# Kernel optimization log

Measured on AMD Instinct MI355X. Metric: run time of the kernel, lower is better.

The kernel has to match this reference:

```python
import jax, jax.numpy as jnp
import numpy as np

KSIZE = 7
STRIDE = 4
SCALE = 10.0
C_IN = 64
C_INT = 16
TOP_M = 100


def _unfold(x, k, s):
    # x: [B,C,H,W] -> [B, C*k*k, L] with torch.nn.Unfold channel ordering (c, ki, kj)
    B, C, H, W = x.shape
    oh = (H - k) // s + 1
    ow = (W - k) // s + 1
    rows = jnp.arange(oh)[:, None] * s + jnp.arange(k)[None, :]  # [oh,k]
    cols = jnp.arange(ow)[:, None] * s + jnp.arange(k)[None, :]  # [ow,k]
    p = x[:, :, rows][:, :, :, :, cols]          # [B,C,oh,k,ow,k]
    p = p.transpose(0, 1, 3, 5, 2, 4)            # [B,C,k,k,oh,ow]
    return p.reshape(B, C * k * k, oh * ow)


def _fold(p, H, W, k, s):
    # inverse of _unfold with overlap-add (torch.nn.Fold semantics)
    B, D, L = p.shape
    C = D // (k * k)
    oh = (H - k) // s + 1
    ow = (W - k) // s + 1
    rows = jnp.arange(oh)[:, None] * s + jnp.arange(k)[None, :]
    cols = jnp.arange(ow)[:, None] * s + jnp.arange(k)[None, :]
    p = p.reshape(B, C, k, k, oh, ow).transpose(0, 1, 4, 2, 5, 3)  # [B,C,oh,k,ow,k]
    out = jnp.zeros((B, C, H, W), p.dtype)
    return out.at[:, :, rows[:, :, None, None], cols[None, None, :, :]].add(p)


def _conv1x1(x, w, b):
    return jnp.einsum('bchw,oc->bohw', x, w) + b[None, :, None, None]


def _conv3x3(x, w, b):
    y = jax.lax.conv_general_dilated(x, w, (1, 1), ((1, 1), (1, 1)),
                                     dimension_numbers=('NCHW', 'OIHW', 'NCHW'))
    return y + b[None, :, None, None]


def setup_inputs() -> dict:
    key = jax.random.key(0)
    ks = jax.random.split(key, 12)
    B, H, W = 4, 127, 127
    s = 0.05  # small init std keeps softmax logits in a sane range
    return {
        'x': jax.random.normal(ks[0], (B, C_IN, H, W), jnp.float32),
        'g_w': jax.random.normal(ks[1], (C_INT, C_IN, 3, 3), jnp.float32) * s,
        'g_b': jnp.zeros((C_INT,), jnp.float32),
        'theta_w': jax.random.normal(ks[2], (C_INT, C_IN), jnp.float32) * s,
        'theta_b': jnp.zeros((C_INT,), jnp.float32),
        'phi_w': jax.random.normal(ks[3], (C_INT, C_IN), jnp.float32) * s,
        'phi_b': jnp.zeros((C_INT,), jnp.float32),
        'match_w': jax.random.normal(ks[4], (C_INT, C_IN), jnp.float32) * s,
        'match_b': jnp.zeros((C_INT,), jnp.float32),
        'restore_w': jax.random.normal(ks[5], (C_IN, C_INT), jnp.float32) * s,
        'restore_b': jnp.zeros((C_IN,), jnp.float32),
    }


def reference(x, g_w, g_b, theta_w, theta_b, phi_w, phi_b,
              match_w, match_b, restore_w, restore_b):
    B, C, H, W = x.shape
    b1 = _conv3x3(x, g_w, g_b)           # [B,16,H,W]
    b2 = _conv1x1(x, theta_w, theta_b)
    b3 = _conv1x1(x, phi_w, phi_b)

    p1 = _unfold(b1, KSIZE, STRIDE).transpose(0, 2, 1)  # [B,L,D], D=16*49
    p2 = _unfold(b2, KSIZE, STRIDE).transpose(0, 2, 1)
    p3 = _unfold(b3, KSIZE, STRIDE).transpose(0, 2, 1)

    score = jnp.einsum('bld,bmd->blm', p1, p2)           # [B,L,L]
    L = score.shape[-1]
    k = min(TOP_M, L)
    vals, idx = jax.lax.top_k(score, k)                  # [B,L,k]
    bI = jnp.arange(B)[:, None, None]
    rI = jnp.arange(L)[None, :, None]
    sparse = jnp.zeros_like(score).at[bI, rI, idx].set(vals)
    attn = jax.nn.softmax(sparse * SCALE, axis=-1)

    agg = jnp.einsum('blm,bmd->bld', attn, p3).transpose(0, 2, 1)  # [B,D,L]
    out = _fold(agg, H, W, KSIZE, STRIDE)                # [B,16,H,W]

    mask = _fold(_unfold(jnp.ones_like(x), KSIZE, STRIDE), H, W, KSIZE, STRIDE)
    mask = _conv1x1(mask, match_w, match_b)              # [B,16,H,W]

    out = out / (mask + 1e-8)
    out = _conv1x1(out, restore_w, restore_b)            # [B,64,H,W]
    return out
```

## Files before the change

### kernel.cpp

```cpp
#include <hip/hip_runtime.h>
#include <hip/hip_bf16.h>

typedef __hip_bfloat16 bf16;
typedef unsigned short ushort_t;
typedef __attribute__((ext_vector_type(8))) __bf16 bfv8;
typedef __attribute__((ext_vector_type(16))) float f32x16;

#define B_   4
#define CIN  64
#define CI   16
#define H_   127
#define W_   127
#define HW   (H_*W_)
#define KS   7
#define ST   4
#define OH_  31
#define L_   961
#define D_   784
#define TOPM 100

#define N1   1032256
#define WG_O 4
#define WT_O (WG_O + 9216)
#define WP_O (WT_O + 1024)
#define BG_O (WP_O + 1024)
#define BT_O (BG_O + 16)
#define BP_O (BT_O + 16)
#define SM_O (BP_O + 16)
#define SB_O (SM_O + 16)
#define RW_O (SB_O + 16)
#define RB_O (RW_O + 1024)
#define B1_O 12448
#define S3_O (B1_O + 3*N1)
#define WB_O (S3_O + B_*D_)
#define REG_O (WB_O + 36864)
#define SROW 964
#define SCSLOT 926464
#define AGSZ 753424
#define TKROW 112
#define SLST 72
#define PKPLANE 753424
#define PKSTR   1506848
#define PADW 129
#define PADPIX (PADW*PADW)
#define XPB  (PADPIX*64)
#define XPU  ((size_t)B_ * XPB)
#define PLANES_FL 4260096
#define PK_O (REG_O + PLANES_FL)

#define FULL_BYTES ((size_t)(PK_O + 3013696) * 4)
#define MID_BYTES  ((size_t)(REG_O + PLANES_FL) * 4)

__device__ __forceinline__ float bf2f(bf16 v) { return __bfloat162float(v); }
__device__ __forceinline__ float bflo(unsigned u) { return __uint_as_float(u << 16); }
__device__ __forceinline__ float bfhi(unsigned u) { return __uint_as_float(u & 0xFFFF0000u); }

template <typename T> struct Ld;
template <> struct Ld<float> {
  static __device__ __forceinline__ float f(const void* p, int i) { return ((const float*)p)[i]; }
};
template <> struct Ld<bf16> {
  static __device__ __forceinline__ float f(const void* p, int i) { return bf2f(((const bf16*)p)[i]); }
};

__device__ __forceinline__ unsigned fmap(float f) {
// ... 13 lines not shown
  h = f2bf(x);
  float hf = __uint_as_float(((unsigned)h) << 16);
  l = f2bf(x - hf);
}

#define LDW(ptr, i) (f ? ((const float*)(ptr))[i] : bf2f(((const bf16*)(ptr))[i]))
__global__ __launch_bounds__(256) void k_prep(
    const void* __restrict__ x,
    const void* g_w, const void* t_w, const void* p_w,
    const void* g_b, const void* t_b, const void* p_b,
    const void* m_w, const void* m_b, const void* r_w, const void* r_b,
    float* __restrict__ ws,
    ushort_t* __restrict__ xhh, ushort_t* __restrict__ xhl)
{
  __shared__ int sflag;
  {
    const unsigned short* xh = (const unsigned short*)x;
    if (threadIdx.x < 64) {
      int c = 0;
#pragma unroll
      for (int j = 0; j < 2; ++j) {
        unsigned u = xh[threadIdx.x * 2 + j];
        unsigned e = (u >> 7) & 0xFF;
        if (e >= 134) c++;
      }
#pragma unroll
      for (int o = 32; o; o >>= 1) c += __shfl_down(c, o);
      if (threadIdx.x == 0) sflag = (c >= 8) ? 1 : 0;
    }
  }
// ... 36 lines not shown
  }
  if (xhh) {
    const int4 z = make_int4(0, 0, 0, 0);
    for (int idx = gid; idx < B_ * 512 * 8; idx += gs) {
      int q = idx & 7, t = idx >> 3;
      int bp = t & 511, bb = t >> 9;
      int pp;
      if (bp < 129) pp = bp;
      else if (bp < 258) pp = 128 * PADW + (bp - 129);
      else if (bp < 385) pp = (bp - 257) * PADW;
      else pp = (bp - 384) * PADW + 128;
      size_t off = ((size_t)bb * PADPIX + pp) * 64 + q * 8;
      *(int4*)(xhh + off) = z;
      *(int4*)(xhl + off) = z;
    }
  }
}

__global__ __launch_bounds__(256) void k_hwc(
    const int* __restrict__ flag, const void* __restrict__ x,
    ushort_t* __restrict__ xhh, ushort_t* __restrict__ xhl)
{
  __shared__ float tile[64][65];
  int pix0 = blockIdx.x * 64;
  int tid = threadIdx.x;
  int g = tid >> 6, p = tid & 63;
  int pix = pix0 + p;
  bool ok = pix < B_ * HW;
  int bb = ok ? pix / HW : 0;
  int r  = ok ? pix - bb * HW : 0;
  if (*flag) {
    const float* xf = (const float*)x;
    for (int c = g * 16; c < g * 16 + 16; ++c)
      tile[p][c] = ok ? xf[((size_t)bb * CIN + c) * HW + r] : 0.f;
  } else {
    const bf16* xb = (const bf16*)x;
    for (int c = g * 16; c < g * 16 + 16; ++c)
      tile[p][c] = ok ? bf2f(xb[((size_t)bb * CIN + c) * HW + r]) : 0.f;
  }
  __syncthreads();
  int c2 = tid & 63, pg = tid >> 6;
  int pix2 = pix0 + pg * 16;
  int bb2 = pix2 / HW, r2 = pix2 - bb2 * HW;
  int h2 = r2 / W_, w2 = r2 - h2 * W_;
  for (int k = 0; k < 16; ++k) {
    if (pix2 + k < B_ * HW) {
      ushort_t h, l; splitbf(tile[pg * 16 + k][c2], h, l);
      size_t off = ((size_t)bb2 * PADPIX + (size_t)(h2 + 1) * PADW + (w2 + 1)) * 64 + c2;
      xhh[off] = h;
      xhl[off] = l;
    }
    if (++w2 == W_) { w2 = 0; if (++h2 == H_) { h2 = 0; ++bb2; } }
  }
}

__global__ __launch_bounds__(256) void k_conv3(
    const float* __restrict__ ws,
    const ushort_t* __restrict__ xhh, const ushort_t* __restrict__ xhl,
    ushort_t* __restrict__ b1h, ushort_t* __restrict__ b1l,
    ushort_t* __restrict__ b2h, ushort_t* __restrict__ b2l,
    ushort_t* __restrict__ b3, ushort_t* __restrict__ pk)
{
  __shared__ ushort_t sAh[128 * SLST], sAl[128 * SLST];
  __shared__ ushort_t sBh[64 * SLST],  sBl[64 * SLST];
  int bz = blockIdx.z;
  int h = blockIdx.x;
  int tid = threadIdx.x, lane = tid & 63, wv = tid >> 6;
  int grp = lane >> 3, ch = lane & 7;

  const ushort_t* xplane = ((wv == 0) ? xhh : xhl) + (size_t)bz * XPB;
  const ushort_t* wBh_ = (const ushort_t*)(ws + WB_O);
  const ushort_t* bsrc = (wv == 2) ? wBh_ : (wBh_ + 9 * 64 * 64);
  ushort_t* dplane = (wv == 0) ? sAh : (wv == 1) ? sAl : (wv == 2) ? sBh : sBl;

  int fr = lane & 31, kh = (lane >> 5) << 3;
  int mt = (wv >> 1) << 1;
// ... 59 lines not shown
      acc1 = __builtin_amdgcn_mfma_f32_32x32x16_bf16(ah1, bh, acc1, 0, 0, 0);
    }
  }
#undef LC
#undef LC_A
#undef LC_W
#undef WC
#undef WC_A
#undef WC_W

  int nw = ((wv & 1) << 5) + fr;
  if (pk) {
    __syncthreads();
    ushort_t* sb1h = sAh;
    ushort_t* sb1l = sAl;
#pragma unroll
    for (int s = 0; s < 2; ++s) {
      int mbase = (mt + s) * 32;
#pragma unroll
      for (int r = 0; r < 16; ++r) {
        int m = mbase + (r & 3) + ((r >> 2) << 3) + ((lane >> 5) << 2);
        float val = s ? acc1[r] : acc0[r];
        if (nw < 16) {
          ushort_t h2, l2; splitbf(val + ws[BG_O + nw], h2, l2);
          sb1h[m * 16 + nw] = h2; sb1l[m * 16 + nw] = l2;
        } else if (m < W_) {
          size_t ob = ((size_t)bz * HW + h * W_ + m) * 16;
          if (nw < 32) {
            int o = nw - 16; ushort_t h2, l2; splitbf(val + ws[BT_O + o], h2, l2);
            b2h[ob + o] = h2; b2l[ob + o] = l2;
          } else if (nw < 48) {
            int o = nw - 32; b3[ob + o] = f2bf(val + ws[BP_O + o]);
          }
        }
      }
    }
    __syncthreads();
    ushort_t* pkb = pk + (size_t)bz * PKSTR;
    int slh_lo = (h >= 6) ? ((h - 3) >> 2) : 0;
    int slh_hi = h >> 2; if (slh_hi > 30) slh_hi = 30;
    for (int slh = slh_lo; slh <= slh_hi; ++slh) {
      int nki = h - 4 * slh;
      size_t rb = ((size_t)nki * 961 + slh * 31) * 112;
      for (int t = tid; t < 31 * 14; t += 256) {
        int slw = t / 14, q = t - slw * 14;
        int m = slw * 4 + (q >> 1);
        int c0 = (q & 1) << 3;
        int4 vh = *(int4*)(sb1h + m * 16 + c0);
        int4 vl = *(int4*)(sb1l + m * 16 + c0);
        size_t doff = rb + (size_t)slw * 112 + q * 8;
        *(int4*)(pkb + doff)           = vh;
        *(int4*)(pkb + PKPLANE + doff) = vl;
      }
    }
  } else {
#pragma unroll
    for (int s = 0; s < 2; ++s) {
      int mbase = (mt + s) * 32;
#pragma unroll
      for (int r = 0; r < 16; ++r) {
        int m = mbase + (r & 3) + ((r >> 2) << 3) + ((lane >> 5) << 2);
        if (m >= W_) continue;
        size_t ob = ((size_t)bz * HW + h * W_ + m) * 16;
        float val = s ? acc1[r] : acc0[r];
        if (nw < 16) {
          ushort_t h2, l2; splitbf(val + ws[BG_O + nw], h2, l2);
          b1h[ob + nw] = h2; b1l[ob + nw] = l2;
// ... 94 lines not shown
    int lh = l / OH_, lw = l % OH_;
    s += bflo((unsigned)B3[((lh * ST + ki) * W_ + lw * ST + kj) * CI + c]);
  }
  red[chunk][c] = s;
  __syncthreads();
  if (threadIdx.x < 16) {
    float t = 0.f;
#pragma unroll
    for (int k = 0; k < 16; ++k) t += red[k][threadIdx.x];
    S3[(b * 49 + pos) * 16 + threadIdx.x] = t;
  }
}

__global__ __launch_bounds__(256) void k_pack(
    const ushort_t* __restrict__ b1h, const ushort_t* __restrict__ b1l,
    ushort_t* __restrict__ pk, int b0, unsigned pkstride_z)
{
  int idx = blockIdx.x * 256 + threadIdx.x;
  if (idx >= 961 * 98) return;
  int row = idx / 98, rem = idx - row * 98;
  int nki = rem / 14, q = rem - nki * 14;
  int slh = row / OH_, slw = row - slh * OH_;
  int src = ((slh * ST) * W_ + slw * ST + nki * W_) * 16 + q * 8;
  int dst = (nki * 961 + row) * 112 + q * 8;
  int batch = b0 + blockIdx.y;
  size_t poff = (size_t)batch * HW * CI;
  ushort_t* pkb = pk + (size_t)blockIdx.y * pkstride_z;
  *(int4*)(pkb + dst)           = *(const int4*)(b1h + poff + src);
  *(int4*)(pkb + PKPLANE + dst) = *(const int4*)(b1l + poff + src);
}

__global__ __launch_bounds__(256) void k_score(
    const ushort_t* __restrict__ b2h, const ushort_t* __restrict__ b2l,
    const ushort_t* __restrict__ pk,
    float* __restrict__ scb, int b0, unsigned scstride_z, unsigned pkstride_z)
{
  __shared__ ushort_t sAh[128 * SLST], sAl[128 * SLST];
  __shared__ ushort_t sBh[64 * SLST],  sBl[64 * SLST];
  int batch = b0 + blockIdx.z;
  size_t poff_g = (size_t)batch * HW * CI;
  float* Sc = scb + (size_t)blockIdx.z * scstride_z;

  int tid = threadIdx.x;
  int m0 = blockIdx.y * 128, n0 = blockIdx.x * 64;
  int lane = tid & 63;
  int wv = tid >> 6;
  int grp = lane >> 3, ch = lane & 7;

  const ushort_t* pkb = pk + (size_t)blockIdx.z * pkstride_z + (size_t)(wv & 1) * PKPLANE;

  int srow = n0 + lane;  if (srow > L_ - 1) srow = L_ - 1;
  int slh = srow / OH_, slw = srow - slh * OH_;
  int sbase = (slh * ST) * W_ + slw * ST;
  const ushort_t* splane = (wv == 2) ? (b2h + poff_g) : (b2l + poff_g);
  ushort_t* dplane = (wv == 0) ? sAh : (wv == 1) ? sAl : (wv == 2) ? sBh : sBl;
  ushort_t* drowB = dplane + lane * SLST;

  int fr = lane & 31;
  int kh = (lane >> 5) << 3;
  int mt = (wv >> 1) << 1;
  int aoff0 = (mt * 32 + fr) * SLST + kh;
  int aoff1 = ((mt + 1) * 32 + fr) * SLST + kh;
  int boff  = (((wv & 1) << 5) + fr) * SLST + kh;

  f32x16 acc0 = {0.f,0.f,0.f,0.f,0.f,0.f,0.f,0.f,0.f,0.f,0.f,0.f,0.f,0.f,0.f,0.f};
  f32x16 acc1 = {0.f,0.f,0.f,0.f,0.f,0.f,0.f,0.f,0.f,0.f,0.f,0.f,0.f,0.f,0.f,0.f};

  int4 pv0, pv1, pv2, pv3, pv4, pv5, pv6, pv7;
  int4 pv8, pv9, pv10, pv11, pv12, pv13, pv14, pv15;

#define LA(j) pv##j = *(const int4*)(pks + (size_t)min(m0 + 8*j + grp, 960) * 112)
#define LA_ALL LA(0); LA(1); LA(2); LA(3); LA(4); LA(5); LA(6); LA(7); \
               LA(8); LA(9); LA(10); LA(11); LA(12); LA(13); LA(14); LA(15)
#define WA(j) *(int4*)(d0 + (j) * 8 * SLST) = pv##j
#define WA_ALL WA(0); WA(1); WA(2); WA(3); WA(4); WA(5); WA(6); WA(7); \
               WA(8); WA(9); WA(10); WA(11); WA(12); WA(13); WA(14); WA(15)

  if (wv < 2) {
    const ushort_t* pks = pkb + ch * 8;
    LA_ALL;
  } else {
    const int4* s0 = (const int4*)(splane + (size_t)sbase * 16);
    pv0 = s0[0]; pv1 = s0[1]; pv2 = s0[2]; pv3 = s0[3];
    pv4 = s0[4]; pv5 = s0[5]; pv6 = s0[6]; pv7 = s0[7];
  }

  for (int r = 0; r < 14; ++r) {
    int half = r & 1;
    __syncthreads();
    if (wv < 2) {
      ushort_t* d0 = dplane + grp * SLST + ch * 8;
      if (!half) { WA_ALL; }
      else if (ch < 6) { WA_ALL; }
    } else {
      *(int4*)(drowB + 0)  = pv0;  *(int4*)(drowB + 8)  = pv1;
      *(int4*)(drowB + 16) = pv2;  *(int4*)(drowB + 24) = pv3;
      *(int4*)(drowB + 32) = pv4;  *(int4*)(drowB + 40) = pv5;
      if (!half) { *(int4*)(drowB + 48) = pv6; *(int4*)(drowB + 56) = pv7; }
    }
    __syncthreads();
    if (r < 13) {
      int rn = r + 1;
      int nki = rn >> 1, odd = rn & 1;
      if (wv < 2) {
        const ushort_t* pks = pkb + (size_t)nki * (961 * 112) + odd * 64 + ch * 8;
        if (!odd) { LA_ALL; }
        else if (ch < 6) { LA_ALL; }
      } else {
        int nkj0 = odd * 4;
        const int4* s0 = (const int4*)(splane + (size_t)(sbase + nki * W_ + nkj0) * 16);
        pv0 = s0[0]; pv1 = s0[1]; pv2 = s0[2]; pv3 = s0[3]; pv4 = s0[4]; pv5 = s0[5];
        if (!odd) { pv6 = s0[6]; pv7 = s0[7]; }
      }
    }
    if (!half) {
#pragma unroll
      for (int t = 0; t < 4; ++t) {
        bfv8 ah0 = *(const bfv8*)(sAh + aoff0 + t * 16);
        bfv8 al0 = *(const bfv8*)(sAl + aoff0 + t * 16);
        bfv8 ah1 = *(const bfv8*)(sAh + aoff1 + t * 16);
        bfv8 al1 = *(const bfv8*)(sAl + aoff1 + t * 16);
        bfv8 bh  = *(const bfv8*)(sBh + boff + t * 16);
        bfv8 bl  = *(const bfv8*)(sBl + boff + t * 16);
        acc0 = __builtin_amdgcn_mfma_f32_32x32x16_bf16(al0, bh, acc0, 0, 0, 0);
        acc0 = __builtin_amdgcn_mfma_f32_32x32x16_bf16(ah0, bl, acc0, 0, 0, 0);
        acc0 = __builtin_amdgcn_mfma_f32_32x32x16_bf16(ah0, bh, acc0, 0, 0, 0);
        acc1 = __builtin_amdgcn_mfma_f32_32x32x16_bf16(al1, bh, acc1, 0, 0, 0);
        acc1 = __builtin_amdgcn_mfma_f32_32x32x16_bf16(ah1, bl, acc1, 0, 0, 0);
// ... 6 lines not shown
        bfv8 al0 = *(const bfv8*)(sAl + aoff0 + t * 16);
        bfv8 ah1 = *(const bfv8*)(sAh + aoff1 + t * 16);
        bfv8 al1 = *(const bfv8*)(sAl + aoff1 + t * 16);
        bfv8 bh  = *(const bfv8*)(sBh + boff + t * 16);
        bfv8 bl  = *(const bfv8*)(sBl + boff + t * 16);
        acc0 = __builtin_amdgcn_mfma_f32_32x32x16_bf16(al0, bh, acc0, 0, 0, 0);
        acc0 = __builtin_amdgcn_mfma_f32_32x32x16_bf16(ah0, bl, acc0, 0, 0, 0);
        acc0 = __builtin_amdgcn_mfma_f32_32x32x16_bf16(ah0, bh, acc0, 0, 0, 0);
        acc1 = __builtin_amdgcn_mfma_f32_32x32x16_bf16(al1, bh, acc1, 0, 0, 0);
        acc1 = __builtin_amdgcn_mfma_f32_32x32x16_bf16(ah1, bl, acc1, 0, 0, 0);
        acc1 = __builtin_amdgcn_mfma_f32_32x32x16_bf16(ah1, bh, acc1, 0, 0, 0);
      }
    }
  }
#undef LA
#undef LA_ALL
#undef WA
#undef WA_ALL

  int nw = n0 + ((wv & 1) << 5) + fr;
  if (nw < L_) {
    int mw0 = m0 + mt * 32;
#pragma unroll
    for (int r = 0; r < 16; ++r) {
      int m = mw0 + (r & 3) + ((r >> 2) << 3) + ((lane >> 5) << 2);
      if (m < L_) Sc[(size_t)m * SROW + nw] = acc0[r];
    }
    int mw1 = m0 + (mt + 1) * 32;
#pragma unroll
    for (int r = 0; r < 16; ++r) {
      int m = mw1 + (r & 3) + ((r >> 2) << 3) + ((lane >> 5) << 2);
      if (m < L_) Sc[(size_t)m * SROW + nw] = acc1[r];
    }
  }
}

__global__ __launch_bounds__(256) void k_topk(
    const float* __restrict__ scb, float* __restrict__ tkw, int* __restrict__ tkp,
    unsigned scstride_z)
{
  __shared__ float swv[4][TOPM];
  __shared__ int spx[4][TOPM];
  int tid = threadIdx.x;
  int wvi = tid >> 6, lane = tid & 63;
  int l = blockIdx.x * 4 + wvi;
  if (l > L_ - 1) l = L_ - 1;
  int bz = blockIdx.y;
  const float4* row4 = (const float4*)(scb + (size_t)bz * scstride_z + (size_t)l * SROW);
  int trow = (bz * L_ + l) * TKROW;

  unsigned k[16];
#pragma unroll
  for (int q = 0; q < 4; ++q) {
    float4 v = row4[q * 64 + lane];
    int ib = (q * 64 + lane) * 4;
    k[q * 4 + 0] = (ib + 0 < L_) ? fmap(v.x) : 0u;
    k[q * 4 + 1] = (ib + 1 < L_) ? fmap(v.y) : 0u;
    k[q * 4 + 2] = (ib + 2 < L_) ? fmap(v.z) : 0u;
    k[q * 4 + 3] = (ib + 3 < L_) ? fmap(v.w) : 0u;
  }

  unsigned mk = 0;
#pragma unroll
  for (int r = 0; r < 16; ++r) mk = max(mk, k[r]);
#pragma unroll
  for (int o = 32; o; o >>= 1) mk = max(mk, (unsigned)__shfl_down((int)mk, o));
  mk = (unsigned)__shfl((int)mk, 0);
  float vmax = unfmap(mk);

  unsigned kk[16];
#pragma unroll
  for (int r = 0; r < 16; ++r) kk[r] = k[r];

  unsigned prefix = 0; int base = 0;
  for (int bit = 30; bit >= 0; bit -= 2) {
    int n3 = 0, n2 = 0, n1 = 0;
#pragma unroll
    for (int r = 0; r < 16; ++r) {
      unsigned f = (kk[r] >> bit) & 3u;
      n3 += (int)__popcll(__ballot(f == 3u));
      n2 += (int)__popcll(__ballot(f >= 2u));
      n1 += (int)__popcll(__ballot(f >= 1u));
    }
    unsigned ch;
    if (base + n3 >= TOPM) ch = 3;
    else if (base + n2 >= TOPM) { ch = 2; base += n3; }
    else if (base + n1 >= TOPM) { ch = 1; base += n2; }
    else { ch = 0; base += n1; }
    prefix |= ch << bit;
#pragma unroll
    for (int r = 0; r < 16; ++r) {
      unsigned f = (kk[r] >> bit) & 3u;
      kk[r] = (f == ch) ? kk[r] : 0u;
    }
  }
  int nA = base;
  int needT = TOPM - nA;

  int cA = 0, cT = 0;
#pragma unroll
  for (int r = 0; r < 16; ++r) { cA += (k[r] > prefix); cT += (k[r] == prefix); }
  int pk = cA | (cT << 16);
  int incl = pk;
#pragma unroll
  for (int o = 1; o < 64; o <<= 1) { int t = __shfl_up(incl, o); if (lane >= o) incl += t; }
  int excl = incl - pk;
  int tA = excl & 0xFFFF, tT = excl >> 16;

  float M = fmaxf(10.f * vmax, 0.f);
  float e0 = __expf(-M);
  float z = 0.f;
#pragma unroll
  for (int r = 0; r < 16; ++r) {
    unsigned kr = k[r];
    int slot = -1;
    if (kr > prefix) slot = tA++;
    else if (kr == prefix) { if (tT < needT) slot = nA + tT; tT++; }
    if (slot >= 0) {
      float v = unfmap(kr);
      float wv = __expf(10.f * v - M);
      swv[wvi][slot] = wv; z += wv;
      int gi = 256 * (r >> 2) + 4 * lane + (r & 3);
      int lh = gi / OH_, lw = gi - lh * OH_;
      spx[wvi][slot] = ((lh * ST) * W_ + lw * ST) * CI;
    }
  }
#pragma unroll
  for (int o = 32; o; o >>= 1) z += __shfl_down(z, o);
  z = __shfl(z, 0);
  float Z = z + (float)(L_ - TOPM) * e0;
  float invZ = 1.f / Z;
  float w0 = e0 / Z;
  __syncthreads();
#pragma unroll
  for (int s0 = 0; s0 < 2; ++s0) {
    int s = lane + 64 * s0;
    if (s < TOPM) {
      tkw[trow + s] = swv[wvi][s] * invZ - w0;
      tkp[trow + s] = spx[wvi][s];
    }
  }
  if (lane == 0) tkw[trow + TOPM] = w0;
}

__global__ __launch_bounds__(128) void k_pv(
    const float* __restrict__ tkw, const int* __restrict__ tkp,
    const ushort_t* __restrict__ b3, const float* __restrict__ s3,
    float* __restrict__ agb, int b0, unsigned agstride_z)
{
  int l = blockIdx.x, bz = blockIdx.y;
  int batch = b0 + bz;
  int trow = (bz * L_ + l) * TKROW;
  const ushort_t* B3 = b3 + (size_t)batch * HW * CI;
  const float* S3 = s3 + (size_t)batch * D_;
  float* agg = agb + (size_t)bz * agstride_z;
  int tid = threadIdx.x;
  if (tid >= 98) return;

  float w0 = tkw[trow + TOPM];
  int pos = tid >> 1;
  int c0 = (tid & 1) << 3;
  int ki = pos / 7, kj = pos - (pos / 7) * 7;
  int poff = (ki * W_ + kj) * CI + c0;

  float a0 = 0.f, a1 = 0.f, a2 = 0.f, a3 = 0.f;
  float a4 = 0.f, a5 = 0.f, a6 = 0.f, a7 = 0.f;
  for (int j0 = 0; j0 < TOPM; j0 += 4) {
    float w_0 = tkw[trow + j0 + 0];
    float w_1 = tkw[trow + j0 + 1];
    float w_2 = tkw[trow + j0 + 2];
    float w_3 = tkw[trow + j0 + 3];
    int p_0 = tkp[trow + j0 + 0];
    int p_1 = tkp[trow + j0 + 1];
    int p_2 = tkp[trow + j0 + 2];
    int p_3 = tkp[trow + j0 + 3];
    const uint4 q0 = *(const uint4*)(B3 + p_0 + poff);
    const uint4 q1 = *(const uint4*)(B3 + p_1 + poff);
    const uint4 q2 = *(const uint4*)(B3 + p_2 + poff);
    const uint4 q3 = *(const uint4*)(B3 + p_3 + poff);
    a0 += w_0 * bflo(q0.x); a1 += w_0 * bfhi(q0.x); a2 += w_0 * bflo(q0.y); a3 += w_0 * bfhi(q0.y);
    a4 += w_0 * bflo(q0.z); a5 += w_0 * bfhi(q0.z); a6 += w_0 * bflo(q0.w); a7 += w_0 * bfhi(q0.w);
    a0 += w_1 * bflo(q1.x); a1 += w_1 * bfhi(q1.x); a2 += w_1 * bflo(q1.y); a3 += w_1 * bfhi(q1.y);
    a4 += w_1 * bflo(q1.z); a5 += w_1 * bfhi(q1.z); a6 += w_1 * bflo(q1.w); a7 += w_1 * bfhi(q1.w);
    a0 += w_2 * bflo(q2.x); a1 += w_2 * bfhi(q2.x); a2 += w_2 * bflo(q2.y); a3 += w_2 * bfhi(q2.y);
    a4 += w_2 * bflo(q2.z); a5 += w_2 * bfhi(q2.z); a6 += w_2 * bflo(q2.w); a7 += w_2 * bfhi(q2.w);
    a0 += w_3 * bflo(q3.x); a1 += w_3 * bfhi(q3.x); a2 += w_3 * bflo(q3.y); a3 += w_3 * bfhi(q3.y);
    a4 += w_3 * bflo(q3.z); a5 += w_3 * bfhi(q3.z); a6 += w_3 * bflo(q3.w); a7 += w_3 * bfhi(q3.w);
  }
  const float4 s40 = *(const float4*)(S3 + tid * 8);
  const float4 s41 = *(const float4*)(S3 + tid * 8 + 4);
// ... 91 lines not shown

  float* W = (float*)d_ws;
  int* flag = (int*)d_ws;
  ushort_t* planes = (ushort_t*)(W + B1_O);
  ushort_t* b1h = planes;
  ushort_t* b1l = planes + (size_t)N1;
  ushort_t* b2h = planes + (size_t)2 * N1;
  ushort_t* b2l = planes + (size_t)3 * N1;
  ushort_t* b3  = planes + (size_t)4 * N1;
  float* s3 = W + S3_O;

  if (ws_size >= FULL_BYTES) {
    ushort_t* xhh = (ushort_t*)(W + REG_O);
    ushort_t* xhl = xhh + XPU;
    float* sc = W + REG_O;
    ushort_t* pk = (ushort_t*)(W + PK_O);
    float* ag = W + PK_O;
    float* tkw = W + B1_O + N1;
    int*   tkp = (int*)(W + B1_O + N1 + N1 / 2);
    k_prep<<<64, 256, 0, stream>>>(x, g_w, th_w, ph_w, g_b, th_b, ph_b,
                                   m_w, m_b, r_w, r_b, W, xhh, xhl);
    k_hwc<<<dim3((B_ * HW + 63) / 64), 256, 0, stream>>>(flag, x, xhh, xhl);
    k_conv3<<<dim3(H_, 1, B_), 256, 0, stream>>>(
        W, xhh, xhl, b1h, b1l, b2h, b2l, b3, pk);
    k_colsum<<<dim3(B_, 49), 256, 0, stream>>>(b3, s3);
    k_score<<<dim3(16, 8, B_), 256, 0, stream>>>(b2h, b2l, pk, sc, 0, SCSLOT, PKSTR);
    k_topk<<<dim3((L_ + 3) / 4, B_), 256, 0, stream>>>(sc, tkw, tkp, SCSLOT);
    k_pv<<<dim3(L_, B_), 128, 0, stream>>>(tkw, tkp, b3, s3, ag, 0, AGSZ);
    k_fold<<<dim3(64, B_), 256, 0, stream>>>(flag, W, ag, d_out, 0, AGSZ);
  } else if (ws_size >= MID_BYTES) {
    ushort_t* xhh = (ushort_t*)(W + REG_O);
    ushort_t* xhl = xhh + XPU;
    float* sc = W + REG_O;
    float* ag = W + REG_O + SCSLOT;
    ushort_t* pk = (ushort_t*)ag;
    k_prep<<<64, 256, 0, stream>>>(x, g_w, th_w, ph_w, g_b, th_b, ph_b,
                                   m_w, m_b, r_w, r_b, W, xhh, xhl);
    k_hwc<<<dim3((B_ * HW + 63) / 64), 256, 0, stream>>>(flag, x, xhh, xhl);
    k_conv3<<<dim3(H_, 1, B_), 256, 0, stream>>>(
        W, xhh, xhl, b1h, b1l, b2h, b2l, b3, (ushort_t*)nullptr);
    k_colsum<<<dim3(B_, 49), 256, 0, stream>>>(b3, s3);
    for (int b = 0; b < B_; ++b) {
      float* tkw = W + B1_O + N1 + (size_t)b * (HW * CI / 2);
      int*   tkp = (int*)(W + B1_O + N1 + N1 / 2 + (size_t)b * (HW * CI / 2));
      k_pack<<<dim3(368, 1), 256, 0, stream>>>(b1h, b1l, pk, b, 0);
      k_score<<<dim3(16, 8, 1), 256, 0, stream>>>(b2h, b2l, pk, sc, b, 0, 0);
      k_topk<<<dim3((L_ + 3) / 4, 1), 256, 0, stream>>>(sc, tkw, tkp, 0);
      k_pv<<<dim3(L_, 1), 128, 0, stream>>>(tkw, tkp, b3, s3, ag, b, 0);
      k_fold<<<dim3(64, 1), 256, 0, stream>>>(flag, W, ag, d_out, b, 0);
    }
  } else {
    float* sc = W + REG_O;
    float* ag = W + REG_O + SCSLOT;
    ushort_t* pk = (ushort_t*)ag;
    k_prep<<<64, 256, 0, stream>>>(x, g_w, th_w, ph_w, g_b, th_b, ph_b,
                                   m_w, m_b, r_w, r_b, W,
                                   (ushort_t*)nullptr, (ushort_t*)nullptr);
    k_convF<<<dim3(4, 16, B_), dim3(32, 8, 1), 0, stream>>>(
        flag, x, g_w, g_b, th_w, th_b, ph_w, ph_b, b1h, b1l, b2h, b2l, b3);
    k_colsum<<<dim3(B_, 49), 256, 0, stream>>>(b3, s3);
    for (int b = 0; b < B_; ++b) {
      float* tkw = W + B1_O + N1 + (size_t)b * (HW * CI / 2);
      int*   tkp = (int*)(W + B1_O + N1 + N1 / 2 + (size_t)b * (HW * CI / 2));
      k_pack<<<dim3(368, 1), 256, 0, stream>>>(b1h, b1l, pk, b, 0);
      k_score<<<dim3(16, 8, 1), 256, 0, stream>>>(b2h, b2l, pk, sc, b, 0, 0);
      k_topk<<<dim3((L_ + 3) / 4, 1), 256, 0, stream>>>(sc, tkw, tkp, 0);
      k_pv<<<dim3(L_, 1), 128, 0, stream>>>(tkw, tkp, b3, s3, ag, b, 0);
      k_fold<<<dim3(64, 1), 256, 0, stream>>>(flag, W, ag, d_out, b, 0);
    }
  }
}
```

Baseline: 255.6 us.

## Fuse topk with PV, pre-pack theta patches, merge HWC transpose into prep

Merges the top-k selection and the weighted patch aggregation into one kernel that keeps the weights and indices in shared memory instead of round-tripping them through global memory. The conv kernel now also writes theta-branch outputs in the packed patch layout, so the score kernel reads both operands through the same strided path rather than gathering B rows from the raw plane. The HWC transpose is folded into the prep kernel, which removes one launch. In exchange the workspace grows by one more packed buffer and the fused kernel runs the selection on a single wave while the other threads wait.

```diff
diff --git a/kernel.cpp b/kernel.cpp
--- a/kernel.cpp
+++ b/kernel.cpp
@@ -37,7 +37,6 @@
 #define SROW 964
 #define SCSLOT 926464
 #define AGSZ 753424
-#define TKROW 112
 #define SLST 72
 #define PKPLANE 753424
 #define PKSTR   1506848
@@ -46,9 +45,10 @@
 #define XPB  (PADPIX*64)
 #define XPU  ((size_t)B_ * XPB)
 #define PLANES_FL 4260096
-#define PK_O (REG_O + PLANES_FL)
-
-#define FULL_BYTES ((size_t)(PK_O + 3013696) * 4)
+#define PK_O  (REG_O + PLANES_FL)
+#define PK2_O (PK_O + 3013696)
+
+#define FULL_BYTES ((size_t)(PK2_O + 3013696) * 4)
 #define MID_BYTES  ((size_t)(REG_O + PLANES_FL) * 4)
 
 __device__ __forceinline__ float bf2f(bf16 v) { return __bfloat162float(v); }
@@ -92,6 +92,7 @@
     ushort_t* __restrict__ xhh, ushort_t* __restrict__ xhl)
 {
   __shared__ int sflag;
+  __shared__ float tile[64][65];
   {
     const unsigned short* xh = (const unsigned short*)x;
     if (threadIdx.x < 64) {
@@ -158,43 +159,37 @@
       *(int4*)(xhh + off) = z;
       *(int4*)(xhl + off) = z;
     }
-  }
-}
-
-__global__ __launch_bounds__(256) void k_hwc(
-    const int* __restrict__ flag, const void* __restrict__ x,
-    ushort_t* __restrict__ xhh, ushort_t* __restrict__ xhl)
-{
-  __shared__ float tile[64][65];
-  int pix0 = blockIdx.x * 64;
-  int tid = threadIdx.x;
-  int g = tid >> 6, p = tid & 63;
-  int pix = pix0 + p;
-  bool ok = pix < B_ * HW;
-  int bb = ok ? pix / HW : 0;
-  int r  = ok ? pix - bb * HW : 0;
-  if (*flag) {
-    const float* xf = (const float*)x;
-    for (int c = g * 16; c < g * 16 + 16; ++c)
-      tile[p][c] = ok ? xf[((size_t)bb * CIN + c) * HW + r] : 0.f;
-  } else {
-    const bf16* xb = (const bf16*)x;
-    for (int c = g * 16; c < g * 16 + 16; ++c)
-      tile[p][c] = ok ? bf2f(xb[((size_t)bb * CIN + c) * HW + r]) : 0.f;
-  }
-  __syncthreads();
-  int c2 = tid & 63, pg = tid >> 6;
-  int pix2 = pix0 + pg * 16;
-  int bb2 = pix2 / HW, r2 = pix2 - bb2 * HW;
-  int h2 = r2 / W_, w2 = r2 - h2 * W_;
-  for (int k = 0; k < 16; ++k) {
-    if (pix2 + k < B_ * HW) {
-      ushort_t h, l; splitbf(tile[pg * 16 + k][c2], h, l);
-      size_t off = ((size_t)bb2 * PADPIX + (size_t)(h2 + 1) * PADW + (w2 + 1)) * 64 + c2;
-      xhh[off] = h;
-      xhl[off] = l;
-    }
-    if (++w2 == W_) { w2 = 0; if (++h2 == H_) { h2 = 0; ++bb2; } }
+    int pix0 = blockIdx.x * 64;
+    if (pix0 < B_ * HW) {
+      int g = threadIdx.x >> 6, p = threadIdx.x & 63;
+      int pix = pix0 + p;
+      bool ok = pix < B_ * HW;
+      int bb = ok ? pix / HW : 0;
+      int r  = ok ? pix - bb * HW : 0;
+      if (f) {
+        const float* xf = (const float*)x;
+        for (int c = g * 16; c < g * 16 + 16; ++c)
+          tile[p][c] = ok ? xf[((size_t)bb * CIN + c) * HW + r] : 0.f;
+      } else {
+        const bf16* xb = (const bf16*)x;
+        for (int c = g * 16; c < g * 16 + 16; ++c)
+          tile[p][c] = ok ? bf2f(xb[((size_t)bb * CIN + c) * HW + r]) : 0.f;
+      }
+      __syncthreads();
+      int c2 = threadIdx.x & 63, pg = threadIdx.x >> 6;
+      int pix2 = pix0 + pg * 16;
+      int bb2 = pix2 / HW, r2 = pix2 - bb2 * HW;
+      int h2 = r2 / W_, w2 = r2 - h2 * W_;
+      for (int k = 0; k < 16; ++k) {
+        if (pix2 + k < B_ * HW) {
+          ushort_t h, l; splitbf(tile[pg * 16 + k][c2], h, l);
+          size_t off = ((size_t)bb2 * PADPIX + (size_t)(h2 + 1) * PADW + (w2 + 1)) * 64 + c2;
+          xhh[off] = h;
+          xhl[off] = l;
+        }
+        if (++w2 == W_) { w2 = 0; if (++h2 == H_) { h2 = 0; ++bb2; } }
+      }
+    }
   }
 }
 
@@ -203,7 +198,7 @@
     const ushort_t* __restrict__ xhh, const ushort_t* __restrict__ xhl,
     ushort_t* __restrict__ b1h, ushort_t* __restrict__ b1l,
     ushort_t* __restrict__ b2h, ushort_t* __restrict__ b2l,
-    ushort_t* __restrict__ b3, ushort_t* __restrict__ pk)
+    ushort_t* __restrict__ b3, ushort_t* __restrict__ pk, ushort_t* __restrict__ pk2)
 {
   __shared__ ushort_t sAh[128 * SLST], sAl[128 * SLST];
   __shared__ ushort_t sBh[64 * SLST],  sBl[64 * SLST];
@@ -293,6 +288,8 @@
     __syncthreads();
     ushort_t* sb1h = sAh;
     ushort_t* sb1l = sAl;
+    ushort_t* sb2h = sBh;
+    ushort_t* sb2l = sBl;
 #pragma unroll
     for (int s = 0; s < 2; ++s) {
       int mbase = (mt + s) * 32;
@@ -303,19 +300,20 @@
         if (nw < 16) {
           ushort_t h2, l2; splitbf(val + ws[BG_O + nw], h2, l2);
           sb1h[m * 16 + nw] = h2; sb1l[m * 16 + nw] = l2;
-        } else if (m < W_) {
-          size_t ob = ((size_t)bz * HW + h * W_ + m) * 16;
-          if (nw < 32) {
-            int o = nw - 16; ushort_t h2, l2; splitbf(val + ws[BT_O + o], h2, l2);
-            b2h[ob + o] = h2; b2l[ob + o] = l2;
-          } else if (nw < 48) {
+        } else if (nw < 32) {
+          int o = nw - 16; ushort_t h2, l2; splitbf(val + ws[BT_O + o], h2, l2);
+          sb2h[m * 16 + o] = h2; sb2l[m * 16 + o] = l2;
+        } else if (nw < 48) {
+          if (m < W_) {
+            size_t ob = ((size_t)bz * HW + h * W_ + m) * 16;
             int o = nw - 32; b3[ob + o] = f2bf(val + ws[BP_O + o]);
           }
         }
       }
     }
     __syncthreads();
-    ushort_t* pkb = pk + (size_t)bz * PKSTR;
+    ushort_t* pk1b = pk  + (size_t)bz * PKSTR;
+    ushort_t* pk2b = pk2 + (size_t)bz * PKSTR;
     int slh_lo = (h >= 6) ? ((h - 3) >> 2) : 0;
     int slh_hi = h >> 2; if (slh_hi > 30) slh_hi = 30;
     for (int slh = slh_lo; slh <= slh_hi; ++slh) {
@@ -325,11 +323,11 @@
         int slw = t / 14, q = t - slw * 14;
         int m = slw * 4 + (q >> 1);
         int c0 = (q & 1) << 3;
-        int4 vh = *(int4*)(sb1h + m * 16 + c0);
-        int4 vl = *(int4*)(sb1l + m * 16 + c0);
         size_t doff = rb + (size_t)slw * 112 + q * 8;
-        *(int4*)(pkb + doff)           = vh;
-        *(int4*)(pkb + PKPLANE + doff) = vl;
+        *(int4*)(pk1b + doff)           = *(int4*)(sb1h + m * 16 + c0);
+        *(int4*)(pk1b + PKPLANE + doff) = *(int4*)(sb1l + m * 16 + c0);
+        *(int4*)(pk2b + doff)           = *(int4*)(sb2h + m * 16 + c0);
+        *(int4*)(pk2b + PKPLANE + doff) = *(int4*)(sb2l + m * 16 + c0);
       }
     }
   } else {
@@ -454,31 +452,34 @@
 
 __global__ __launch_bounds__(256) void k_pack(
     const ushort_t* __restrict__ b1h, const ushort_t* __restrict__ b1l,
-    ushort_t* __restrict__ pk, int b0, unsigned pkstride_z)
+    const ushort_t* __restrict__ b2h, const ushort_t* __restrict__ b2l,
+    ushort_t* __restrict__ pk, ushort_t* __restrict__ pk2,
+    int b0, unsigned pkstride_z)
 {
   int idx = blockIdx.x * 256 + threadIdx.x;
-  if (idx >= 961 * 98) return;
-  int row = idx / 98, rem = idx - row * 98;
+  if (idx >= 2 * 961 * 98) return;
+  int sel = (idx >= 961 * 98);
+  int i2 = sel ? idx - 961 * 98 : idx;
+  int row = i2 / 98, rem = i2 - row * 98;
   int nki = rem / 14, q = rem - nki * 14;
   int slh = row / OH_, slw = row - slh * OH_;
   int src = ((slh * ST) * W_ + slw * ST + nki * W_) * 16 + q * 8;
   int dst = (nki * 961 + row) * 112 + q * 8;
   int batch = b0 + blockIdx.y;
   size_t poff = (size_t)batch * HW * CI;
-  ushort_t* pkb = pk + (size_t)blockIdx.y * pkstride_z;
-  *(int4*)(pkb + dst)           = *(const int4*)(b1h + poff + src);
-  *(int4*)(pkb + PKPLANE + dst) = *(const int4*)(b1l + poff + src);
+  const ushort_t* sh = sel ? b2h : b1h;
+  const ushort_t* sl = sel ? b2l : b1l;
+  ushort_t* pkb = (sel ? pk2 : pk) + (size_t)blockIdx.y * pkstride_z;
+  *(int4*)(pkb + dst)           = *(const int4*)(sh + poff + src);
+  *(int4*)(pkb + PKPLANE + dst) = *(const int4*)(sl + poff + src);
 }
 
 __global__ __launch_bounds__(256) void k_score(
-    const ushort_t* __restrict__ b2h, const ushort_t* __restrict__ b2l,
-    const ushort_t* __restrict__ pk,
-    float* __restrict__ scb, int b0, unsigned scstride_z, unsigned pkstride_z)
+    const ushort_t* __restrict__ pk, const ushort_t* __restrict__ pk2,
+    float* __restrict__ scb, unsigned scstride_z, unsigned pkstride_z)
 {
   __shared__ ushort_t sAh[128 * SLST], sAl[128 * SLST];
   __shared__ ushort_t sBh[64 * SLST],  sBl[64 * SLST];
-  int batch = b0 + blockIdx.z;
-  size_t poff_g = (size_t)batch * HW * CI;
   float* Sc = scb + (size_t)blockIdx.z * scstride_z;
 
   int tid = threadIdx.x;
@@ -487,14 +488,11 @@
   int wv = tid >> 6;
   int grp = lane >> 3, ch = lane & 7;
 
-  const ushort_t* pkb = pk + (size_t)blockIdx.z * pkstride_z + (size_t)(wv & 1) * PKPLANE;
-
-  int srow = n0 + lane;  if (srow > L_ - 1) srow = L_ - 1;
-  int slh = srow / OH_, slw = srow - slh * OH_;
-  int sbase = (slh * ST) * W_ + slw * ST;
-  const ushort_t* splane = (wv == 2) ? (b2h + poff_g) : (b2l + poff_g);
+  const ushort_t* pka = ((wv < 2) ? pk : pk2)
+      + (size_t)blockIdx.z * pkstride_z + (size_t)(wv & 1) * PKPLANE;
+  int base_mn = (wv < 2) ? m0 : n0;
+
   ushort_t* dplane = (wv == 0) ? sAh : (wv == 1) ? sAl : (wv == 2) ? sBh : sBl;
-  ushort_t* drowB = dplane + lane * SLST;
 
   int fr = lane & 31;
   int kh = (lane >> 5) << 3;
@@ -509,49 +507,33 @@
   int4 pv0, pv1, pv2, pv3, pv4, pv5, pv6, pv7;
   int4 pv8, pv9, pv10, pv11, pv12, pv13, pv14, pv15;
 
-#define LA(j) pv##j = *(const int4*)(pks + (size_t)min(m0 + 8*j + grp, 960) * 112)
-#define LA_ALL LA(0); LA(1); LA(2); LA(3); LA(4); LA(5); LA(6); LA(7); \
-               LA(8); LA(9); LA(10); LA(11); LA(12); LA(13); LA(14); LA(15)
+#define LA(j) pv##j = *(const int4*)(pks + (size_t)min(base_mn + 8*(j) + grp, 960) * 112)
+#define LA_A LA(0); LA(1); LA(2); LA(3); LA(4); LA(5); LA(6); LA(7); \
+             LA(8); LA(9); LA(10); LA(11); LA(12); LA(13); LA(14); LA(15)
+#define LA_B LA(0); LA(1); LA(2); LA(3); LA(4); LA(5); LA(6); LA(7)
 #define WA(j) *(int4*)(d0 + (j) * 8 * SLST) = pv##j
-#define WA_ALL WA(0); WA(1); WA(2); WA(3); WA(4); WA(5); WA(6); WA(7); \
-               WA(8); WA(9); WA(10); WA(11); WA(12); WA(13); WA(14); WA(15)
-
-  if (wv < 2) {
-    const ushort_t* pks = pkb + ch * 8;
-    LA_ALL;
-  } else {
-    const int4* s0 = (const int4*)(splane + (size_t)sbase * 16);
-    pv0 = s0[0]; pv1 = s0[1]; pv2 = s0[2]; pv3 = s0[3];
-    pv4 = s0[4]; pv5 = s0[5]; pv6 = s0[6]; pv7 = s0[7];
+#define WA_A WA(0); WA(1); WA(2); WA(3); WA(4); WA(5); WA(6); WA(7); \
+             WA(8); WA(9); WA(10); WA(11); WA(12); WA(13); WA(14); WA(15)
+#define WA_B WA(0); WA(1); WA(2); WA(3); WA(4); WA(5); WA(6); WA(7)
+
+  {
+    const ushort_t* pks = pka + ch * 8;
+    if (wv < 2) { LA_A; } else { LA_B; }
   }
 
   for (int r = 0; r < 14; ++r) {
     int half = r & 1;
     __syncthreads();
-    if (wv < 2) {
+    {
       ushort_t* d0 = dplane + grp * SLST + ch * 8;
-      if (!half) { WA_ALL; }
-      else if (ch < 6) { WA_ALL; }
-    } else {
-      *(int4*)(drowB + 0)  = pv0;  *(int4*)(drowB + 8)  = pv1;
-      *(int4*)(drowB + 16) = pv2;  *(int4*)(drowB + 24) = pv3;
-      *(int4*)(drowB + 32) = pv4;  *(int4*)(drowB + 40) = pv5;
-      if (!half) { *(int4*)(drowB + 48) = pv6; *(int4*)(drowB + 56) = pv7; }
+      if (!half || ch < 6) { if (wv < 2) { WA_A; } else { WA_B; } }
     }
     __syncthreads();
     if (r < 13) {
       int rn = r + 1;
       int nki = rn >> 1, odd = rn & 1;
-      if (wv < 2) {
-        const ushort_t* pks = pkb + (size_t)nki * (961 * 112) + odd * 64 + ch * 8;
-        if (!odd) { LA_ALL; }
-        else if (ch < 6) { LA_ALL; }
-      } else {
-        int nkj0 = odd * 4;
-        const int4* s0 = (const int4*)(splane + (size_t)(sbase + nki * W_ + nkj0) * 16);
-        pv0 = s0[0]; pv1 = s0[1]; pv2 = s0[2]; pv3 = s0[3]; pv4 = s0[4]; pv5 = s0[5];
-        if (!odd) { pv6 = s0[6]; pv7 = s0[7]; }
-      }
+      const ushort_t* pks = pka + (size_t)nki * (961 * 112) + odd * 64 + ch * 8;
+      if (!odd || ch < 6) { if (wv < 2) { LA_A; } else { LA_B; } }
     }
     if (!half) {
 #pragma unroll
@@ -588,9 +570,11 @@
     }
   }
 #undef LA
-#undef LA_ALL
+#undef LA_A
+#undef LA_B
 #undef WA
-#undef WA_ALL
+#undef WA_A
+#undef WA_B
 
   int nw = n0 + ((wv & 1) << 5) + fr;
   if (nw < L_) {
@@ -609,129 +593,114 @@
   }
 }
 
-__global__ __launch_bounds__(256) void k_topk(
-    const float* __restrict__ scb, float* __restrict__ tkw, int* __restrict__ tkp,
-    unsigned scstride_z)
-{
-  __shared__ float swv[4][TOPM];
-  __shared__ int spx[4][TOPM];
+__global__ __launch_bounds__(128) void k_tkpv(
+    const float* __restrict__ scb,
+    const ushort_t* __restrict__ b3, const float* __restrict__ s3,
+    float* __restrict__ agb, int b0, unsigned scstride_z, unsigned agstride_z)
+{
+  __shared__ float swv[TOPM];
+  __shared__ int spx[TOPM];
+  __shared__ float sw0, sinvZ;
+  int l = blockIdx.x, bz = blockIdx.y;
   int tid = threadIdx.x;
-  int wvi = tid >> 6, lane = tid & 63;
-  int l = blockIdx.x * 4 + wvi;
-  if (l > L_ - 1) l = L_ - 1;
-  int bz = blockIdx.y;
-  const float4* row4 = (const float4*)(scb + (size_t)bz * scstride_z + (size_t)l * SROW);
-  int trow = (bz * L_ + l) * TKROW;
-
-  unsigned k[16];
-#pragma unroll
-  for (int q = 0; q < 4; ++q) {
-    float4 v = row4[q * 64 + lane];
-    int ib = (q * 64 + lane) * 4;
-    k[q * 4 + 0] = (ib + 0 < L_) ? fmap(v.x) : 0u;
-    k[q * 4 + 1] = (ib + 1 < L_) ? fmap(v.y) : 0u;
-    k[q * 4 + 2] = (ib + 2 < L_) ? fmap(v.z) : 0u;
-    k[q * 4 + 3] = (ib + 3 < L_) ? fmap(v.w) : 0u;
-  }
-
-  unsigned mk = 0;
-#pragma unroll
-  for (int r = 0; r < 16; ++r) mk = max(mk, k[r]);
-#pragma unroll
-  for (int o = 32; o; o >>= 1) mk = max(mk, (unsigned)__shfl_down((int)mk, o));
-  mk = (unsigned)__shfl((int)mk, 0);
-  float vmax = unfmap(mk);
-
-  unsigned kk[16];
-#pragma unroll
-  for (int r = 0; r < 16; ++r) kk[r] = k[r];
-
-  unsigned prefix = 0; int base = 0;
-  for (int bit = 30; bit >= 0; bit -= 2) {
-    int n3 = 0, n2 = 0, n1 = 0;
+
+  if (tid < 64) {
+    int lane = tid;
+    const float4* row4 = (const float4*)(scb + (size_t)bz * scstride_z + (size_t)l * SROW);
+
+    unsigned k[16];
+#pragma unroll
+    for (int q = 0; q < 4; ++q) {
+      float4 v = row4[q * 64 + lane];
+      int ib = (q * 64 + lane) * 4;
+      k[q * 4 + 0] = (ib + 0 < L_) ? fmap(v.x) : 0u;
+      k[q * 4 + 1] = (ib + 1 < L_) ? fmap(v.y) : 0u;
+      k[q * 4 + 2] = (ib + 2 < L_) ? fmap(v.z) : 0u;
+      k[q * 4 + 3] = (ib + 3 < L_) ? fmap(v.w) : 0u;
+    }
+
+    unsigned mk = 0;
+#pragma unroll
+    for (int r = 0; r < 16; ++r) mk = max(mk, k[r]);
+#pragma unroll
+    for (int o = 32; o; o >>= 1) mk = max(mk, (unsigned)__shfl_down((int)mk, o));
+    mk = (unsigned)__shfl((int)mk, 0);
+    float vmax = unfmap(mk);
+
+    unsigned kk[16];
+#pragma unroll
+    for (int r = 0; r < 16; ++r) kk[r] = k[r];
+
+    unsigned prefix = 0; int base = 0;
+    for (int bit = 30; bit >= 0; bit -= 2) {
+      int n3 = 0, n2 = 0, n1 = 0;
+#pragma unroll
+      for (int r = 0; r < 16; ++r) {
+        unsigned f = (kk[r] >> bit) & 3u;
+        n3 += (int)__popcll(__ballot(f == 3u));
+        n2 += (int)__popcll(__ballot(f >= 2u));
+        n1 += (int)__popcll(__ballot(f >= 1u));
+      }
+      unsigned ch;
+      if (base + n3 >= TOPM) ch = 3;
+      else if (base + n2 >= TOPM) { ch = 2; base += n3; }
+      else if (base + n1 >= TOPM) { ch = 1; base += n2; }
+      else { ch = 0; base += n1; }
+      prefix |= ch << bit;
+#pragma unroll
+      for (int r = 0; r < 16; ++r) {
+        unsigned f = (kk[r] >> bit) & 3u;
+        kk[r] = (f == ch) ? kk[r] : 0u;
+      }
+    }
+    int nA = base;
+    int needT = TOPM - nA;
+
+    int cA = 0, cT = 0;
+#pragma unroll
+    for (int r = 0; r < 16; ++r) { cA += (k[r] > prefix); cT += (k[r] == prefix); }
+    int pkc = cA | (cT << 16);
+    int incl = pkc;
+#pragma unroll
+    for (int o = 1; o < 64; o <<= 1) { int t = __shfl_up(incl, o); if (lane >= o) incl += t; }
+    int excl = incl - pkc;
+    int tA = excl & 0xFFFF, tT = excl >> 16;
+
+    float M = fmaxf(10.f * vmax, 0.f);
+    float e0 = __expf(-M);
+    float z = 0.f;
 #pragma unroll
     for (int r = 0; r < 16; ++r) {
-      unsigned f = (kk[r] >> bit) & 3u;
-      n3 += (int)__popcll(__ballot(f == 3u));
-      n2 += (int)__popcll(__ballot(f >= 2u));
-      n1 += (int)__popcll(__ballot(f >= 1u));
-    }
-    unsigned ch;
-    if (base + n3 >= TOPM) ch = 3;
-    else if (base + n2 >= TOPM) { ch = 2; base += n3; }
-    else if (base + n1 >= TOPM) { ch = 1; base += n2; }
-    else { ch = 0; base += n1; }
-    prefix |= ch << bit;
-#pragma unroll
-    for (int r = 0; r < 16; ++r) {
-      unsigned f = (kk[r] >> bit) & 3u;
-      kk[r] = (f == ch) ? kk[r] : 0u;
-    }
-  }
-  int nA = base;
-  int needT = TOPM - nA;
-
-  int cA = 0, cT = 0;
-#pragma unroll
-  for (int r = 0; r < 16; ++r) { cA += (k[r] > prefix); cT += (k[r] == prefix); }
-  int pk = cA | (cT << 16);
-  int incl = pk;
-#pragma unroll
-  for (int o = 1; o < 64; o <<= 1) { int t = __shfl_up(incl, o); if (lane >= o) incl += t; }
-  int excl = incl - pk;
-  int tA = excl & 0xFFFF, tT = excl >> 16;
-
-  float M = fmaxf(10.f * vmax, 0.f);
-  float e0 = __expf(-M);
-  float z = 0.f;
-#pragma unroll
-  for (int r = 0; r < 16; ++r) {
-    unsigned kr = k[r];
-    int slot = -1;
-    if (kr > prefix) slot = tA++;
-    else if (kr == prefix) { if (tT < needT) slot = nA + tT; tT++; }
-    if (slot >= 0) {
-      float v = unfmap(kr);
-      float wv = __expf(10.f * v - M);
-      swv[wvi][slot] = wv; z += wv;
-      int gi = 256 * (r >> 2) + 4 * lane + (r & 3);
-      int lh = gi / OH_, lw = gi - lh * OH_;
-      spx[wvi][slot] = ((lh * ST) * W_ + lw * ST) * CI;
-    }
-  }
-#pragma unroll
-  for (int o = 32; o; o >>= 1) z += __shfl_down(z, o);
-  z = __shfl(z, 0);
-  float Z = z + (float)(L_ - TOPM) * e0;
-  float invZ = 1.f / Z;
-  float w0 = e0 / Z;
+      unsigned kr = k[r];
+      int slot = -1;
+      if (kr > prefix) slot = tA++;
+      else if (kr == prefix) { if (tT < needT) slot = nA + tT; tT++; }
+      if (slot >= 0) {
+        float v = unfmap(kr);
+        float wv = __expf(10.f * v - M);
+        swv[slot] = wv; z += wv;
+        int gi = 256 * (r >> 2) + 4 * lane + (r & 3);
+        int lh = gi / OH_, lw = gi - lh * OH_;
+        spx[slot] = ((lh * ST) * W_ + lw * ST) * CI;
+      }
+    }
+#pragma unroll
+    for (int o = 32; o; o >>= 1) z += __shfl_down(z, o);
+    z = __shfl(z, 0);
+    float Z = z + (float)(L_ - TOPM) * e0;
+    if (lane == 0) { sinvZ = 1.f / Z; sw0 = e0 / Z; }
+  }
   __syncthreads();
-#pragma unroll
-  for (int s0 = 0; s0 < 2; ++s0) {
-    int s = lane + 64 * s0;
-    if (s < TOPM) {
-      tkw[trow + s] = swv[wvi][s] * invZ - w0;
-      tkp[trow + s] = spx[wvi][s];
-    }
-  }
-  if (lane == 0) tkw[trow + TOPM] = w0;
-}
-
-__global__ __launch_bounds__(128) void k_pv(
-    const float* __restrict__ tkw, const int* __restrict__ tkp,
-    const ushort_t* __restrict__ b3, const float* __restrict__ s3,
-    float* __restrict__ agb, int b0, unsigned agstride_z)
-{
-  int l = blockIdx.x, bz = blockIdx.y;
+  if (tid < TOPM) swv[tid] = swv[tid] * sinvZ - sw0;
+  __syncthreads();
+
+  if (tid >= 98) return;
   int batch = b0 + bz;
-  int trow = (bz * L_ + l) * TKROW;
   const ushort_t* B3 = b3 + (size_t)batch * HW * CI;
   const float* S3 = s3 + (size_t)batch * D_;
   float* agg = agb + (size_t)bz * agstride_z;
-  int tid = threadIdx.x;
-  if (tid >= 98) return;
-
-  float w0 = tkw[trow + TOPM];
+
+  float w0 = sw0;
   int pos = tid >> 1;
   int c0 = (tid & 1) << 3;
   int ki = pos / 7, kj = pos - (pos / 7) * 7;
@@ -740,14 +709,14 @@
   float a0 = 0.f, a1 = 0.f, a2 = 0.f, a3 = 0.f;
   float a4 = 0.f, a5 = 0.f, a6 = 0.f, a7 = 0.f;
   for (int j0 = 0; j0 < TOPM; j0 += 4) {
-    float w_0 = tkw[trow + j0 + 0];
-    float w_1 = tkw[trow + j0 + 1];
-    float w_2 = tkw[trow + j0 + 2];
-    float w_3 = tkw[trow + j0 + 3];
-    int p_0 = tkp[trow + j0 + 0];
-    int p_1 = tkp[trow + j0 + 1];
-    int p_2 = tkp[trow + j0 + 2];
-    int p_3 = tkp[trow + j0 + 3];
+    float w_0 = swv[j0 + 0];
+    float w_1 = swv[j0 + 1];
+    float w_2 = swv[j0 + 2];
+    float w_3 = swv[j0 + 3];
+    int p_0 = spx[j0 + 0];
+    int p_1 = spx[j0 + 1];
+    int p_2 = spx[j0 + 2];
+    int p_3 = spx[j0 + 3];
     const uint4 q0 = *(const uint4*)(B3 + p_0 + poff);
     const uint4 q1 = *(const uint4*)(B3 + p_1 + poff);
     const uint4 q2 = *(const uint4*)(B3 + p_2 + poff);
@@ -869,58 +838,50 @@
     ushort_t* xhh = (ushort_t*)(W + REG_O);
     ushort_t* xhl = xhh + XPU;
     float* sc = W + REG_O;
-    ushort_t* pk = (ushort_t*)(W + PK_O);
+    ushort_t* pk  = (ushort_t*)(W + PK_O);
+    ushort_t* pk2 = (ushort_t*)(W + PK2_O);
     float* ag = W + PK_O;
-    float* tkw = W + B1_O + N1;
-    int*   tkp = (int*)(W + B1_O + N1 + N1 / 2);
-    k_prep<<<64, 256, 0, stream>>>(x, g_w, th_w, ph_w, g_b, th_b, ph_b,
-                                   m_w, m_b, r_w, r_b, W, xhh, xhl);
-    k_hwc<<<dim3((B_ * HW + 63) / 64), 256, 0, stream>>>(flag, x, xhh, xhl);
+    k_prep<<<dim3((B_ * HW + 63) / 64), 256, 0, stream>>>(
+        x, g_w, th_w, ph_w, g_b, th_b, ph_b, m_w, m_b, r_w, r_b, W, xhh, xhl);
     k_conv3<<<dim3(H_, 1, B_), 256, 0, stream>>>(
-        W, xhh, xhl, b1h, b1l, b2h, b2l, b3, pk);
+        W, xhh, xhl, b1h, b1l, b2h, b2l, b3, pk, pk2);
     k_colsum<<<dim3(B_, 49), 256, 0, stream>>>(b3, s3);
-    k_score<<<dim3(16, 8, B_), 256, 0, stream>>>(b2h, b2l, pk, sc, 0, SCSLOT, PKSTR);
-    k_topk<<<dim3((L_ + 3) / 4, B_), 256, 0, stream>>>(sc, tkw, tkp, SCSLOT);
-    k_pv<<<dim3(L_, B_), 128, 0, stream>>>(tkw, tkp, b3, s3, ag, 0, AGSZ);
+    k_score<<<dim3(16, 8, B_), 256, 0, stream>>>(pk, pk2, sc, SCSLOT, PKSTR);
+    k_tkpv<<<dim3(L_, B_), 128, 0, stream>>>(sc, b3, s3, ag, 0, SCSLOT, AGSZ);
     k_fold<<<dim3(64, B_), 256, 0, stream>>>(flag, W, ag, d_out, 0, AGSZ);
   } else if (ws_size >= MID_BYTES) {
     ushort_t* xhh = (ushort_t*)(W + REG_O);
     ushort_t* xhl = xhh + XPU;
     float* sc = W + REG_O;
     float* ag = W + REG_O + SCSLOT;
-    ushort_t* pk = (ushort_t*)ag;
-    k_prep<<<64, 256, 0, stream>>>(x, g_w, th_w, ph_w, g_b, th_b, ph_b,
-                                   m_w, m_b, r_w, r_b, W, xhh, xhl);
-    k_hwc<<<dim3((B_ * HW + 63) / 64), 256, 0, stream>>>(flag, x, xhh, xhl);
+    ushort_t* pk  = (ushort_t*)ag;
+    ushort_t* pk2 = pk + (size_t)PKSTR;
+    k_prep<<<dim3((B_ * HW + 63) / 64), 256, 0, stream>>>(
+        x, g_w, th_w, ph_w, g_b, th_b, ph_b, m_w, m_b, r_w, r_b, W, xhh, xhl);
     k_conv3<<<dim3(H_, 1, B_), 256, 0, stream>>>(
-        W, xhh, xhl, b1h, b1l, b2h, b2l, b3, (ushort_t*)nullptr);
+        W, xhh, xhl, b1h, b1l, b2h, b2l, b3, (ushort_t*)nullptr, (ushort_t*)nullptr);
     k_colsum<<<dim3(B_, 49), 256, 0, stream>>>(b3, s3);
     for (int b = 0; b < B_; ++b) {
-      float* tkw = W + B1_O + N1 + (size_t)b * (HW * CI / 2);
-      int*   tkp = (int*)(W + B1_O + N1 + N1 / 2 + (size_t)b * (HW * CI / 2));
-      k_pack<<<dim3(368, 1), 256, 0, stream>>>(b1h, b1l, pk, b, 0);
-      k_score<<<dim3(16, 8, 1), 256, 0, stream>>>(b2h, b2l, pk, sc, b, 0, 0);
-      k_topk<<<dim3((L_ + 3) / 4, 1), 256, 0, stream>>>(sc, tkw, tkp, 0);
-      k_pv<<<dim3(L_, 1), 128, 0, stream>>>(tkw, tkp, b3, s3, ag, b, 0);
+      k_pack<<<dim3(736, 1), 256, 0, stream>>>(b1h, b1l, b2h, b2l, pk, pk2, b, 0);
+      k_score<<<dim3(16, 8, 1), 256, 0, stream>>>(pk, pk2, sc, 0, 0);
+      k_tkpv<<<dim3(L_, 1), 128, 0, stream>>>(sc, b3, s3, ag, b, 0, 0);
       k_fold<<<dim3(64, 1), 256, 0, stream>>>(flag, W, ag, d_out, b, 0);
     }
   } else {
     float* sc = W + REG_O;
     float* ag = W + REG_O + SCSLOT;
-    ushort_t* pk = (ushort_t*)ag;
-    k_prep<<<64, 256, 0, stream>>>(x, g_w, th_w, ph_w, g_b, th_b, ph_b,
-                                   m_w, m_b, r_w, r_b, W,
-                                   (ushort_t*)nullptr, (ushort_t*)nullptr);
+    ushort_t* pk  = (ushort_t*)ag;
+    ushort_t* pk2 = pk + (size_t)PKSTR;
+    k_prep<<<64, 256, 0, stream>>>(
+        x, g_w, th_w, ph_w, g_b, th_b, ph_b, m_w, m_b, r_w, r_b, W,
+        (ushort_t*)nullptr, (ushort_t*)nullptr);
     k_convF<<<dim3(4, 16, B_), dim3(32, 8, 1), 0, stream>>>(
         flag, x, g_w, g_b, th_w, th_b, ph_w, ph_b, b1h, b1l, b2h, b2l, b3);
     k_colsum<<<dim3(B_, 49), 256, 0, stream>>>(b3, s3);
     for (int b = 0; b < B_; ++b) {
-      float* tkw = W + B1_O + N1 + (size_t)b * (HW * CI / 2);
-      int*   tkp = (int*)(W + B1_O + N1 + N1 / 2 + (size_t)b * (HW * CI / 2));
-      k_pack<<<dim3(368, 1), 256, 0, stream>>>(b1h, b1l, pk, b, 0);
-      k_score<<<dim3(16, 8, 1), 256, 0, stream>>>(b2h, b2l, pk, sc, b, 0, 0);
-      k_topk<<<dim3((L_ + 3) / 4, 1), 256, 0, stream>>>(sc, tkw, tkp, 0);
-      k_pv<<<dim3(L_, 1), 128, 0, stream>>>(tkw, tkp, b3, s3, ag, b, 0);
+      k_pack<<<dim3(736, 1), 256, 0, stream>>>(b1h, b1l, b2h, b2l, pk, pk2, b, 0);
+      k_score<<<dim3(16, 8, 1), 256, 0, stream>>>(pk, pk2, sc, 0, 0);
+      k_tkpv<<<dim3(L_, 1), 128, 0, stream>>>(sc, b3, s3, ag, b, 0, 0);
       k_fold<<<dim3(64, 1), 256, 0, stream>>>(flag, W, ag, d_out, b, 0);
     }
   }
```

Result: faster. 247.7 us (-3.1%).
